# Performance work log

Measured on AMD Instinct MI355X. Metric: run time of the kernel, lower is better.

Reference implementation:

```python
import jax, jax.numpy as jnp
import numpy as np
import math

EPS = 1e-5
GN_GROUPS = 32


def conv2d(x, w, padding):
    # x: [B,C,H,W], w: [O,I,kh,kw]
    return jax.lax.conv_general_dilated(
        x, w, window_strides=(1, 1), padding=[(padding, padding)] * 2,
        dimension_numbers=("NCHW", "OIHW", "NCHW"))


def group_norm(x, weight, bias, groups=GN_GROUPS, eps=EPS):
    B, C, H, W = x.shape
    xg = x.reshape(B, groups, C // groups, H, W)
    mu = xg.mean(axis=(2, 3, 4), keepdims=True)
    var = xg.var(axis=(2, 3, 4), keepdims=True)
    xn = (xg - mu) * jax.lax.rsqrt(var + eps)
    xn = xn.reshape(B, C, H, W)
    return xn * weight[None, :, None, None] + bias[None, :, None, None]


def setup_inputs() -> dict:
    key = jax.random.key(0)
    ks = jax.random.split(key, 8)
    B, C, H, W = 8, 256, 80, 80
    init_gate = 0.99
    gate_bias_val = 0.5 * math.log((1 + init_gate) / (1 - init_gate))
    return {
        "x": jax.random.normal(ks[0], (B, C, H, W), dtype=jnp.float32),
        "w1": jax.random.normal(ks[1], (C, C, 3, 3), dtype=jnp.float32) * 0.01,
        "gn1_w": jnp.ones((C,), dtype=jnp.float32),
        "gn1_b": jnp.zeros((C,), dtype=jnp.float32),
        "w2": jax.random.normal(ks[2], (C, C, 3, 3), dtype=jnp.float32) * 0.01,
        "gn2_w": jnp.ones((C,), dtype=jnp.float32),
        "gn2_b": jnp.zeros((C,), dtype=jnp.float32),
        "gate_w": jax.random.normal(ks[3], (1, C, 1, 1), dtype=jnp.float32) * 0.01,
        "gate_b": jnp.full((1,), gate_bias_val, dtype=jnp.float32),
    }


def reference(x, w1, gn1_w, gn1_b, w2, gn2_w, gn2_b, gate_w, gate_b):
    # shortcut is identity (in_channels == out_channels, stride 1)
    shortcut = x
    # conv1 -> GN -> ReLU
    h = jax.nn.relu(group_norm(conv2d(x, w1, padding=1), gn1_w, gn1_b))
    # conv2 -> GN
    h = group_norm(conv2d(h, w2, padding=1), gn2_w, gn2_b)
    # SpatialGate: 1x1 conv on the original input, ReTanH activation
    g = conv2d(x, gate_w, padding=0) + gate_b[None, :, None, None]  # [B,1,H,W]
    gate = jnp.clip(jnp.tanh(g), 0.0, None)
    # num_groups == 1: encode/decode are identity reshapes; gate broadcasts over C
    out = h * gate
    return jax.nn.relu(out + shortcut)
```

## Files before the change

### kernel.cpp

```cpp
#include <hip/hip_runtime.h>
#include <math.h>

#define NB   8
#define NC   256
#define NH   80
#define NW   80
#define NHW  6400
#define GN_EPS 1e-5f

typedef __bf16 bf16;
typedef bf16 bf16x2 __attribute__((ext_vector_type(2)));
typedef bf16 bf16x4 __attribute__((ext_vector_type(4)));
typedef bf16 bf16x8 __attribute__((ext_vector_type(8)));
typedef float f32x4 __attribute__((ext_vector_type(4)));

typedef __attribute__((address_space(1))) void gvoid;
typedef __attribute__((address_space(3))) void lvoid;
__device__ __forceinline__ void glds16(const void* g, void* l) {
    __builtin_amdgcn_global_load_lds((const gvoid*)g, (lvoid*)l, 16, 0, 0);
}

#define AW_T 2048

#define PREP_GRID 2048

__global__ __launch_bounds__(256) void prep_kernel(
    const float* __restrict__ x, bf16* __restrict__ xp,
    const float* __restrict__ gw, float* __restrict__ gsum,
    const float* __restrict__ w1, const float* __restrict__ w2,
    bf16* __restrict__ wA1, bf16* __restrict__ wA2, float* __restrict__ stats)
{
    int bid = blockIdx.x;
    int tid = threadIdx.x;
    if (bid >= PREP_GRID) {
        int blk = bid - PREP_GRID;
        if (blk == 0) {
            #pragma unroll
            for (int k = 0; k < 8; k++) stats[tid + k * 256] = 0.0f;
            return;
        }
        __shared__ float lw[32 * 292];
        int rb    = blk - 1;
        int wsel  = rb >> 6;
        int chunk = (rb >> 3) & 7;
        int cog   = rb & 7;
        const float* w = wsel ? w2 : w1;
        bf16* wA       = wsel ? wA2 : wA1;
        const float* src = w + (size_t)cog * 32 * 2304 + chunk * 288;
        for (int v = tid; v < 2304; v += 256) {
            int co = v / 72, f4o = v - co * 72;
            float4 t = *(const float4*)(src + (size_t)co * 2304 + f4o * 4);
            *(float4*)(&lw[co * 292 + f4o * 4]) = t;
        }
        __syncthreads();
        for (int v = tid; v < 1152; v += 256) {
            int seg = v >> 6;
            int off = v & 63;
            int tap = seg >> 1, coqL = seg & 1;
            int qq = off >> 4, n = off & 15;
            int coL = coqL * 16 + n;
            bf16x8 pk;
            #pragma unroll
            for (int j = 0; j < 8; j++) {
                int ciL = qq * 8 + j;
                pk[j] = (bf16)lw[coL * 292 + ciL * 9 + tap];
            }
            size_t oidx = (((size_t)(chunk * 9 + tap) * 16 + cog * 2 + coqL) * 512)
                          + qq * 128 + n * 8;
            *(bf16x8*)(wA + oidx) = pk;
        }
        return;
    }
    __shared__ float tile[8][4][88];
    for (int vb = bid; vb < 5120; vb += PREP_GRID) {
        int rg  = vb % 20;
        int cib = (vb / 20) & 31;
        int b   = vb / 640;
        for (int u = tid; u < 640; u += 256) {
            int c8 = u / 80; int rem = u - c8 * 80;
            int rr = rem / 20; int c4 = rem - rr * 20;
            float4 v = *(const float4*)(
                x + ((size_t)(b * NC + cib * 8 + c8) * NH + rg * 4 + rr) * NW + c4 * 4);
            *(float4*)(&tile[c8][rr][c4 * 4]) = v;
        }
        __syncthreads();
        for (int u = tid; u < 320; u += 256) {
            int rr = u / 80, col = u - rr * 80;
            bf16x8 pk;
            #pragma unroll
            for (int j = 0; j < 8; j++) pk[j] = (bf16)tile[j][rr][col];
            size_t base = (((size_t)(b * 32 + cib) * 82 + rg * 4 + rr + 1) * 82) * 8 + 8;
            *(bf16x8*)(xp + base + col * 8) = pk;
        }
        for (int u = tid; u < 320; u += 256) {
            int rr = u / 80, col = u - rr * 80;
            float s = 0.0f;
            #pragma unroll
            for (int c8 = 0; c8 < 8; c8++)
                s = fmaf(tile[c8][rr][col], gw[cib * 8 + c8], s);
            atomicAdd(&gsum[(size_t)b * NHW + (rg * 4 + rr) * 80 + col], s);
        }
        const uint4 z4 = make_uint4(0u, 0u, 0u, 0u);
        size_t img = ((size_t)(b * 32 + cib)) * 82;
        if (tid < 8) {
            int rr = tid >> 1, col = (tid & 1) * 81;
            *(uint4*)(xp + ((img + rg * 4 + rr + 1) * 82 + col) * 8) = z4;
        }
        if (rg == 0 || rg == 19) {
            int prow = (rg == 0) ? 0 : 81;
            for (int u = tid; u < 82; u += 256)
                *(uint4*)(xp + ((img + prow) * 82 + u) * 8) = z4;
        }
        __syncthreads();
    }
}

__global__ __launch_bounds__(256, 4) void conv_kernel(
    const bf16* __restrict__ xp, const bf16* __restrict__ wA,
    bf16* __restrict__ y, float* __restrict__ ssum, float* __restrict__ ssq)
{
    __shared__ __align__(16) bf16 Aw[9 * AW_T];
    __shared__ float wgs[8], wgq[8];

    int tid  = threadIdx.x;
    int wid  = tid >> 6;
    int lane = tid & 63;
    int n = lane & 15, q = lane >> 4;

    int bid = blockIdx.x;
    int ct  = bid / 160;
    int t   = bid - ct * 160;
    int b   = t / 20;
    int rt  = t - b * 20;
    int co0 = ct * 64, h0 = rt * 4;

    if (tid < 8) { wgs[tid] = 0.0f; wgq[tid] = 0.0f; }

    f32x4 acc[4][5];
    #pragma unroll
    for (int i = 0; i < 4; i++)
        #pragma unroll
        for (int j = 0; j < 5; j++) acc[i][j] = (f32x4){0.f, 0.f, 0.f, 0.f};

    for (int c = 0; c < 8; c++) {
        __syncthreads();
        for (int p = wid; p < 36; p += 4) {
            int tap = p >> 2, mt = p & 3;
            glds16((const char*)(wA + (((size_t)c * 9 + tap) * 16 + ct * 4 + mt) * 512) + lane * 16,
                   (char*)(Aw + tap * AW_T + mt * 512) + lane * 16);
        }
        __syncthreads();

        const bf16* awc = Aw + lane * 8;
        const bf16* xq  = xp + (((size_t)(b * 32 + c * 4 + q) * 82 + (h0 + wid)) * 82) * 8 + n * 8;

        bf16x8 L0[15], L1[15];
        #pragma unroll
        for (int k = 0; k < 15; k++)
            L0[k] = *(const bf16x8*)(xq + ((k / 3) * 16 + (k % 3)) * 8);
        #pragma unroll
        for (int k = 0; k < 15; k++)
            L1[k] = *(const bf16x8*)(xq + (82 + (k / 3) * 16 + (k % 3)) * 8);

        #pragma unroll
        for (int s = 0; s < 3; s++) {
            bf16x8 af[4];
            #pragma unroll
            for (int mt = 0; mt < 4; mt++)
                af[mt] = *(const bf16x8*)(awc + s * AW_T + mt * 512);
            #pragma unroll
            for (int mt = 0; mt < 4; mt++)
                #pragma unroll
                for (int nt = 0; nt < 5; nt++)
                    acc[mt][nt] = __builtin_amdgcn_mfma_f32_16x16x32_bf16(
                        af[mt], L0[nt * 3 + s], acc[mt][nt], 0, 0, 0);
        }
        #pragma unroll
        for (int k = 0; k < 15; k++)
            L0[k] = *(const bf16x8*)(xq + (164 + (k / 3) * 16 + (k % 3)) * 8);

        #pragma unroll
        for (int s = 0; s < 3; s++) {
            bf16x8 af[4];
            #pragma unroll
            for (int mt = 0; mt < 4; mt++)
                af[mt] = *(const bf16x8*)(awc + (3 + s) * AW_T + mt * 512);
            #pragma unroll
            for (int mt = 0; mt < 4; mt++)
                #pragma unroll
                for (int nt = 0; nt < 5; nt++)
                    acc[mt][nt] = __builtin_amdgcn_mfma_f32_16x16x32_bf16(
                        af[mt], L1[nt * 3 + s], acc[mt][nt], 0, 0, 0);
        }
        #pragma unroll
        for (int s = 0; s < 3; s++) {
            bf16x8 af[4];
            #pragma unroll
            for (int mt = 0; mt < 4; mt++)
                af[mt] = *(const bf16x8*)(awc + (6 + s) * AW_T + mt * 512);
            #pragma unroll
            for (int mt = 0; mt < 4; mt++)
                #pragma unroll
                for (int nt = 0; nt < 5; nt++)
                    acc[mt][nt] = __builtin_amdgcn_mfma_f32_16x16x32_bf16(
                        af[mt], L0[nt * 3 + s], acc[mt][nt], 0, 0, 0);
        }
    }

    int h = h0 + wid;
    #pragma unroll
    for (int mt = 0; mt < 4; mt++) {
        float s1 = 0.0f, s2 = 0.0f;
        int co  = co0 + mt * 16 + q * 4;
        int cib = co >> 3, c8 = co & 7;
        #pragma unroll
        for (int nt = 0; nt < 5; nt++) {
            int col = nt * 16 + n;
            bf16x4 pk;
            #pragma unroll
            for (int rg = 0; rg < 4; rg++) {
                float v = acc[mt][nt][rg];
                pk[rg] = (bf16)v;
                s1 += v;
                s2 = fmaf(v, v, s2);
            }
            *(bf16x4*)(y + ((((size_t)(b * 32 + cib) * 80 + h) * 80 + col) * 8 + c8)) = pk;
        }
        #pragma unroll
        for (int off = 1; off < 16; off <<= 1) {
            s1 += __shfl_xor(s1, off, 64);
            s2 += __shfl_xor(s2, off, 64);
        }
        if (n == 0) {
            int gl = mt * 2 + (q >> 1);
            atomicAdd(&wgs[gl], s1);
            atomicAdd(&wgq[gl], s2);
        }
    }
    __syncthreads();
    if (tid < 8) {
        atomicAdd(&ssum[b * 32 + ct * 8 + tid], wgs[tid]);
        atomicAdd(&ssq [b * 32 + ct * 8 + tid], wgq[tid]);
    }
}

__global__ __launch_bounds__(256) void prep2_kernel(
    const bf16* __restrict__ y, bf16* __restrict__ xp,
    const float* __restrict__ s, const float* __restrict__ sq,
    const float* __restrict__ gamma, const float* __restrict__ beta)
{
    int bid = blockIdx.x;
    for (int vb = bid; vb < 5120; vb += PREP_GRID) {
        int b = vb / 640; int rem = vb - b * 640;
        int cib = rem / 20; int rq = rem - cib * 20;
        int gidx = b * 32 + cib;
        const float cnt = (float)(8 * NHW);
        float m  = s[gidx] / cnt;
        float vv = sq[gidx] / cnt - m * m;
        float r  = rsqrtf(vv + GN_EPS);
        float scj[8], shj[8];
        #pragma unroll
        for (int j = 0; j < 8; j++) {
            int c = cib * 8 + j;
            scj[j] = r * gamma[c];
            shj[j] = beta[c] - m * scj[j];
        }
        const bf16* src = y + (size_t)(b * 32 + cib) * 51200 + rq * 2560;
        for (int u = threadIdx.x; u < 320; u += 256) {
            int e = u * 8;
            int row = rq * 4 + e / 640;
            int w640 = e - (e / 640) * 640;
            bf16x8 iv = *(const bf16x8*)(src + e);
            bf16x8 pk;
            #pragma unroll
            for (int j = 0; j < 8; j++)
                pk[j] = (bf16)fmaxf(fmaf((float)iv[j], scj[j], shj[j]), 0.0f);
            size_t xidx = (((size_t)(b * 32 + cib) * 82 + row + 1) * 82) * 8 + 8 + w640;
            *(bf16x8*)(xp + xidx) = pk;
        }
    }
}

__global__ __launch_bounds__(256) void final_kernel(
    const bf16* __restrict__ y, const float* __restrict__ x,
    const float* __restrict__ gsum, const float* __restrict__ gb,
    const float* __restrict__ s, const float* __restrict__ sq,
    const float* __restrict__ gamma, const float* __restrict__ beta,
    float* __restrict__ out)
{
    __shared__ float lds[8 * 328];
    int bid = blockIdx.x;
    float gb0 = gb[0];
    for (int vb = bid; vb < 5120; vb += PREP_GRID) {
        int b = vb / 640; int rem = vb - b * 640;
        int cib = rem / 20; int rq = rem - cib * 20;
        int gidx = b * 32 + cib;
        const float cnt = (float)(8 * NHW);
        float m  = s[gidx] / cnt;
        float vv = sq[gidx] / cnt - m * m;
        float r  = rsqrtf(vv + GN_EPS);
        float scj[8], shj[8];
        #pragma unroll
        for (int j = 0; j < 8; j++) {
            int c = cib * 8 + j;
            scj[j] = r * gamma[c];
            shj[j] = beta[c] - m * scj[j];
        }
        const bf16* src = y + (size_t)(b * 32 + cib) * 51200 + rq * 2560;
        for (int u = threadIdx.x; u < 320; u += 256) {
            bf16x8 iv = *(const bf16x8*)(src + u * 8);
            #pragma unroll
            for (int j = 0; j < 8; j++)
                lds[j * 328 + u] = fmaf((float)iv[j], scj[j], shj[j]);
        }
        __syncthreads();
        const float* gp = gsum + (size_t)b * NHW + rq * 320;
        for (int u = threadIdx.x; u < 640; u += 256) {
            int c8 = u / 80; int rc = (u - c8 * 80) * 4;
            int c = cib * 8 + c8;
            size_t oidx = (size_t)(b * NC + c) * NHW + rq * 320 + rc;
            float4 xv = *(const float4*)(x + oidx);
            float4 gv = *(const float4*)(gp + rc);
            float4 lv = *(const float4*)(&lds[c8 * 328 + rc]);
            float4 ov;
            ov.x = fmaxf(fmaf(lv.x, fmaxf(tanhf(gv.x + gb0), 0.0f), xv.x), 0.0f);
            ov.y = fmaxf(fmaf(lv.y, fmaxf(tanhf(gv.y + gb0), 0.0f), xv.y), 0.0f);
            ov.z = fmaxf(fmaf(lv.z, fmaxf(tanhf(gv.z + gb0), 0.0f), xv.z), 0.0f);
            ov.w = fmaxf(fmaf(lv.w, fmaxf(tanhf(gv.w + gb0), 0.0f), xv.w), 0.0f);
            *(float4*)(out + oidx) = ov;
        }
        __syncthreads();
    }
}

extern "C" void kernel_launch(void* const* d_in, const int* in_sizes, int n_in,
                              void* d_out, int out_size, void* d_ws, size_t ws_size,
                              hipStream_t stream)
{
    const float* x     = (const float*)d_in[0];
    const float* w1    = (const float*)d_in[1];
    const float* gn1_w = (const float*)d_in[2];
    const float* gn1_b = (const float*)d_in[3];
    const float* w2    = (const float*)d_in[4];
    const float* gn2_w = (const float*)d_in[5];
    const float* gn2_b = (const float*)d_in[6];
    const float* gw    = (const float*)d_in[7];
    const float* gb    = (const float*)d_in[8];

    bf16*  xp  = (bf16*)d_out;
    float* out = (float*)d_out;

    char* wsb = (char*)d_ws;
    bf16*  y     = (bf16*)wsb;
    float* gsum  = (float*)(wsb + 26214400);
    bf16*  wA1   = (bf16*)(wsb + 26214400 + 204800);
    bf16*  wA2   = wA1 + 589824;
    float* stats = (float*)(wsb + 26214400 + 204800 + 2 * 1179648);
    float* s1  = stats,        * s1q = stats + 256;
    float* s2  = stats + 1024, * s2q = stats + 1280;

    hipMemsetAsync(gsum, 0, NB * NHW * sizeof(float), stream);

    prep_kernel<<<PREP_GRID + 129, 256, 0, stream>>>(x, xp, gw, gsum, w1, w2, wA1, wA2, stats);
    conv_kernel<<<640, 256, 0, stream>>>(xp, wA1, y, s1, s1q);
    prep2_kernel<<<PREP_GRID, 256, 0, stream>>>(y, xp, s1, s1q, gn1_w, gn1_b);
    conv_kernel<<<640, 256, 0, stream>>>(xp, wA2, y, s2, s2q);
    final_kernel<<<PREP_GRID, 256, 0, stream>>>(y, x, gsum, gb, s2, s2q, gn2_w, gn2_b, out);
}
```

Measured before the change: 277.7 us.

## Fuse GroupNorm epilogues into conv kernels using a software grid barrier

Each conv kernel now keeps its accumulators in registers, publishes GroupNorm partial sums, and waits at a device-wide atomic barrier. After the barrier it reads the final statistics and applies the normalization itself. Conv1 writes ReLU(GN) directly into the padded bf16 input buffer for conv2, and conv2 applies GN, the spatial gate, the residual add and the final ReLU straight to the output. This removes the bf16 intermediate tensor and the separate prep2 and final kernels, saving their global-memory round trips and launches. The cost is that all 640 blocks must be resident at once for the barrier, and the final epilogue uses narrower scalar strided stores and loads.

New measurement: 725.4 us. 161% more time.

```diff
diff --git a/kernel.cpp b/kernel.cpp
--- a/kernel.cpp
+++ b/kernel.cpp
@@ -18,6 +18,31 @@
 typedef __attribute__((address_space(3))) void lvoid;
 __device__ __forceinline__ void glds16(const void* g, void* l) {
     __builtin_amdgcn_global_load_lds((const gvoid*)g, (lvoid*)l, 16, 0, 0);
+}
+
+__device__ __forceinline__ void grid_barrier(unsigned* bar, unsigned nblk) {
+    __syncthreads();
+    if (threadIdx.x == 0) {
+        unsigned gen = __hip_atomic_load(&bar[1], __ATOMIC_RELAXED,
+                                         __HIP_MEMORY_SCOPE_AGENT);
+        unsigned prev = __hip_atomic_fetch_add(&bar[0], 1u, __ATOMIC_ACQ_REL,
+                                               __HIP_MEMORY_SCOPE_AGENT);
+        if (prev == nblk - 1u) {
+            __hip_atomic_store(&bar[0], 0u, __ATOMIC_RELAXED,
+                               __HIP_MEMORY_SCOPE_AGENT);
+            __hip_atomic_fetch_add(&bar[1], 1u, __ATOMIC_ACQ_REL,
+                                   __HIP_MEMORY_SCOPE_AGENT);
+        } else {
+            while (__hip_atomic_load(&bar[1], __ATOMIC_ACQUIRE,
+                                     __HIP_MEMORY_SCOPE_AGENT) == gen)
+                __builtin_amdgcn_s_sleep(1);
+        }
+    }
+    __syncthreads();
+}
+
+__device__ __forceinline__ float aload(const float* p) {
+    return __hip_atomic_load(p, __ATOMIC_RELAXED, __HIP_MEMORY_SCOPE_AGENT);
 }
 
 #define AW_T 2048
@@ -115,12 +140,16 @@
     }
 }
 
-__global__ __launch_bounds__(256, 4) void conv_kernel(
-    const bf16* __restrict__ xp, const bf16* __restrict__ wA,
-    bf16* __restrict__ y, float* __restrict__ ssum, float* __restrict__ ssq)
+__global__ __launch_bounds__(256, 4) void conv1_fused(
+    bf16* xp, const bf16* __restrict__ wA,
+    float* __restrict__ ssum, float* __restrict__ ssq,
+    const float* __restrict__ gamma, const float* __restrict__ beta,
+    unsigned* bar)
 {
     __shared__ __align__(16) bf16 Aw[9 * AW_T];
     __shared__ float wgs[8], wgq[8];
+    __shared__ float gm[8], gr[8];
+    __shared__ float lgam[64], lbet[64];
 
     int tid  = threadIdx.x;
     int wid  = tid >> 6;
@@ -135,6 +164,7 @@
     int co0 = ct * 64, h0 = rt * 4;
 
     if (tid < 8) { wgs[tid] = 0.0f; wgq[tid] = 0.0f; }
+    if (tid < 64) { lgam[tid] = gamma[co0 + tid]; lbet[tid] = beta[co0 + tid]; }
 
     f32x4 acc[4][5];
     #pragma unroll
@@ -207,25 +237,17 @@
         }
     }
 
-    int h = h0 + wid;
     #pragma unroll
     for (int mt = 0; mt < 4; mt++) {
         float s1 = 0.0f, s2 = 0.0f;
-        int co  = co0 + mt * 16 + q * 4;
-        int cib = co >> 3, c8 = co & 7;
-        #pragma unroll
-        for (int nt = 0; nt < 5; nt++) {
-            int col = nt * 16 + n;
-            bf16x4 pk;
+        #pragma unroll
+        for (int nt = 0; nt < 5; nt++)
             #pragma unroll
             for (int rg = 0; rg < 4; rg++) {
                 float v = acc[mt][nt][rg];
-                pk[rg] = (bf16)v;
                 s1 += v;
                 s2 = fmaf(v, v, s2);
             }
-            *(bf16x4*)(y + ((((size_t)(b * 32 + cib) * 80 + h) * 80 + col) * 8 + c8)) = pk;
-        }
         #pragma unroll
         for (int off = 1; off < 16; off <<= 1) {
             s1 += __shfl_xor(s1, off, 64);
@@ -242,94 +264,212 @@
         atomicAdd(&ssum[b * 32 + ct * 8 + tid], wgs[tid]);
         atomicAdd(&ssq [b * 32 + ct * 8 + tid], wgq[tid]);
     }
-}
-
-__global__ __launch_bounds__(256) void prep2_kernel(
-    const bf16* __restrict__ y, bf16* __restrict__ xp,
-    const float* __restrict__ s, const float* __restrict__ sq,
-    const float* __restrict__ gamma, const float* __restrict__ beta)
+
+    grid_barrier(bar, 640);
+
+    const float cnt = (float)(8 * NHW);
+    if (tid < 8) {
+        float s  = aload(&ssum[b * 32 + ct * 8 + tid]);
+        float q2 = aload(&ssq [b * 32 + ct * 8 + tid]);
+        float m = s / cnt;
+        gm[tid] = m;
+        gr[tid] = rsqrtf(q2 / cnt - m * m + GN_EPS);
+    }
+    __syncthreads();
+
+    int h = h0 + wid;
+    #pragma unroll
+    for (int mt = 0; mt < 4; mt++) {
+        int gl = mt * 2 + (q >> 1);
+        float m = gm[gl], r = gr[gl];
+        int cL  = mt * 16 + q * 4;
+        int cib = ct * 8 + gl;
+        int c8  = (q * 4) & 7;
+        float sc[4], sh[4];
+        #pragma unroll
+        for (int rg = 0; rg < 4; rg++) {
+            sc[rg] = r * lgam[cL + rg];
+            sh[rg] = lbet[cL + rg] - m * sc[rg];
+        }
+        #pragma unroll
+        for (int nt = 0; nt < 5; nt++) {
+            int col = nt * 16 + n;
+            bf16x4 pk;
+            #pragma unroll
+            for (int rg = 0; rg < 4; rg++)
+                pk[rg] = (bf16)fmaxf(fmaf(acc[mt][nt][rg], sc[rg], sh[rg]), 0.0f);
+            *(bf16x4*)(xp + (((size_t)(b * 32 + cib) * 82 + h + 1) * 82) * 8 + 8 + col * 8 + c8) = pk;
+        }
+    }
+}
+
+__global__ __launch_bounds__(256, 4) void conv2_fused(
+    const bf16* __restrict__ xp, const bf16* __restrict__ wA,
+    const float* __restrict__ x, const float* __restrict__ gsum,
+    const float* __restrict__ gb,
+    float* __restrict__ ssum, float* __restrict__ ssq,
+    const float* __restrict__ gamma, const float* __restrict__ beta,
+    float* __restrict__ out, unsigned* bar)
 {
+    __shared__ __align__(16) bf16 Aw[9 * AW_T];
+    __shared__ float wgs[8], wgq[8];
+    __shared__ float gm[8], gr[8];
+    __shared__ float lgam[64], lbet[64];
+
+    int tid  = threadIdx.x;
+    int wid  = tid >> 6;
+    int lane = tid & 63;
+    int n = lane & 15, q = lane >> 4;
+
     int bid = blockIdx.x;
-    for (int vb = bid; vb < 5120; vb += PREP_GRID) {
-        int b = vb / 640; int rem = vb - b * 640;
-        int cib = rem / 20; int rq = rem - cib * 20;
-        int gidx = b * 32 + cib;
-        const float cnt = (float)(8 * NHW);
-        float m  = s[gidx] / cnt;
-        float vv = sq[gidx] / cnt - m * m;
-        float r  = rsqrtf(vv + GN_EPS);
-        float scj[8], shj[8];
-        #pragma unroll
-        for (int j = 0; j < 8; j++) {
-            int c = cib * 8 + j;
-            scj[j] = r * gamma[c];
-            shj[j] = beta[c] - m * scj[j];
-        }
-        const bf16* src = y + (size_t)(b * 32 + cib) * 51200 + rq * 2560;
-        for (int u = threadIdx.x; u < 320; u += 256) {
-            int e = u * 8;
-            int row = rq * 4 + e / 640;
-            int w640 = e - (e / 640) * 640;
-            bf16x8 iv = *(const bf16x8*)(src + e);
-            bf16x8 pk;
-            #pragma unroll
-            for (int j = 0; j < 8; j++)
-                pk[j] = (bf16)fmaxf(fmaf((float)iv[j], scj[j], shj[j]), 0.0f);
-            size_t xidx = (((size_t)(b * 32 + cib) * 82 + row + 1) * 82) * 8 + 8 + w640;
-            *(bf16x8*)(xp + xidx) = pk;
-        }
-    }
-}
-
-__global__ __launch_bounds__(256) void final_kernel(
-    const bf16* __restrict__ y, const float* __restrict__ x,
-    const float* __restrict__ gsum, const float* __restrict__ gb,
-    const float* __restrict__ s, const float* __restrict__ sq,
-    const float* __restrict__ gamma, const float* __restrict__ beta,
-    float* __restrict__ out)
-{
-    __shared__ float lds[8 * 328];
-    int bid = blockIdx.x;
+    int ct  = bid / 160;
+    int t   = bid - ct * 160;
+    int b   = t / 20;
+    int rt  = t - b * 20;
+    int co0 = ct * 64, h0 = rt * 4;
+
+    if (tid < 8) { wgs[tid] = 0.0f; wgq[tid] = 0.0f; }
+    if (tid < 64) { lgam[tid] = gamma[co0 + tid]; lbet[tid] = beta[co0 + tid]; }
+
+    f32x4 acc[4][5];
+    #pragma unroll
+    for (int i = 0; i < 4; i++)
+        #pragma unroll
+        for (int j = 0; j < 5; j++) acc[i][j] = (f32x4){0.f, 0.f, 0.f, 0.f};
+
+    for (int c = 0; c < 8; c++) {
+        __syncthreads();
+        for (int p = wid; p < 36; p += 4) {
+            int tap = p >> 2, mt = p & 3;
+            glds16((const char*)(wA + (((size_t)c * 9 + tap) * 16 + ct * 4 + mt) * 512) + lane * 16,
+                   (char*)(Aw + tap * AW_T + mt * 512) + lane * 16);
+        }
+        __syncthreads();
+
+        const bf16* awc = Aw + lane * 8;
+        const bf16* xq  = xp + (((size_t)(b * 32 + c * 4 + q) * 82 + (h0 + wid)) * 82) * 8 + n * 8;
+
+        bf16x8 L0[15], L1[15];
+        #pragma unroll
+        for (int k = 0; k < 15; k++)
+            L0[k] = *(const bf16x8*)(xq + ((k / 3) * 16 + (k % 3)) * 8);
+        #pragma unroll
+        for (int k = 0; k < 15; k++)
+            L1[k] = *(const bf16x8*)(xq + (82 + (k / 3) * 16 + (k % 3)) * 8);
+
+        #pragma unroll
+        for (int s = 0; s < 3; s++) {
+            bf16x8 af[4];
+            #pragma unroll
+            for (int mt = 0; mt < 4; mt++)
+                af[mt] = *(const bf16x8*)(awc + s * AW_T + mt * 512);
+            #pragma unroll
+            for (int mt = 0; mt < 4; mt++)
+                #pragma unroll
+                for (int nt = 0; nt < 5; nt++)
+                    acc[mt][nt] = __builtin_amdgcn_mfma_f32_16x16x32_bf16(
+                        af[mt], L0[nt * 3 + s], acc[mt][nt], 0, 0, 0);
+        }
+        #pragma unroll
+        for (int k = 0; k < 15; k++)
+            L0[k] = *(const bf16x8*)(xq + (164 + (k / 3) * 16 + (k % 3)) * 8);
+
+        #pragma unroll
+        for (int s = 0; s < 3; s++) {
+            bf16x8 af[4];
+            #pragma unroll
+            for (int mt = 0; mt < 4; mt++)
+                af[mt] = *(const bf16x8*)(awc + (3 + s) * AW_T + mt * 512);
+            #pragma unroll
+            for (int mt = 0; mt < 4; mt++)
+                #pragma unroll
+                for (int nt = 0; nt < 5; nt++)
+                    acc[mt][nt] = __builtin_amdgcn_mfma_f32_16x16x32_bf16(
+                        af[mt], L1[nt * 3 + s], acc[mt][nt], 0, 0, 0);
+        }
+        #pragma unroll
+        for (int s = 0; s < 3; s++) {
+            bf16x8 af[4];
+            #pragma unroll
+            for (int mt = 0; mt < 4; mt++)
+                af[mt] = *(const bf16x8*)(awc + (6 + s) * AW_T + mt * 512);
+            #pragma unroll
+            for (int mt = 0; mt < 4; mt++)
+                #pragma unroll
+                for (int nt = 0; nt < 5; nt++)
+                    acc[mt][nt] = __builtin_amdgcn_mfma_f32_16x16x32_bf16(
+                        af[mt], L0[nt * 3 + s], acc[mt][nt], 0, 0, 0);
+        }
+    }
+
+    #pragma unroll
+    for (int mt = 0; mt < 4; mt++) {
+        float s1 = 0.0f, s2 = 0.0f;
+        #pragma unroll
+        for (int nt = 0; nt < 5; nt++)
+            #pragma unroll
+            for (int rg = 0; rg < 4; rg++) {
+                float v = acc[mt][nt][rg];
+                s1 += v;
+                s2 = fmaf(v, v, s2);
+            }
+        #pragma unroll
+        for (int off = 1; off < 16; off <<= 1) {
+            s1 += __shfl_xor(s1, off, 64);
+            s2 += __shfl_xor(s2, off, 64);
+        }
+        if (n == 0) {
+            int gl = mt * 2 + (q >> 1);
+            atomicAdd(&wgs[gl], s1);
+            atomicAdd(&wgq[gl], s2);
+        }
+    }
+    __syncthreads();
+    if (tid < 8) {
+        atomicAdd(&ssum[b * 32 + ct * 8 + tid], wgs[tid]);
+        atomicAdd(&ssq [b * 32 + ct * 8 + tid], wgq[tid]);
+    }
+
+    grid_barrier(bar, 640);
+
+    const float cnt = (float)(8 * NHW);
+    if (tid < 8) {
+        float s  = aload(&ssum[b * 32 + ct * 8 + tid]);
+        float q2 = aload(&ssq [b * 32 + ct * 8 + tid]);
+        float m = s / cnt;
+        gm[tid] = m;
+        gr[tid] = rsqrtf(q2 / cnt - m * m + GN_EPS);
+    }
+    __syncthreads();
+
+    int h = h0 + wid;
     float gb0 = gb[0];
-    for (int vb = bid; vb < 5120; vb += PREP_GRID) {
-        int b = vb / 640; int rem = vb - b * 640;
-        int cib = rem / 20; int rq = rem - cib * 20;
-        int gidx = b * 32 + cib;
-        const float cnt = (float)(8 * NHW);
-        float m  = s[gidx] / cnt;
-        float vv = sq[gidx] / cnt - m * m;
-        float r  = rsqrtf(vv + GN_EPS);
-        float scj[8], shj[8];
-        #pragma unroll
-        for (int j = 0; j < 8; j++) {
-            int c = cib * 8 + j;
-            scj[j] = r * gamma[c];
-            shj[j] = beta[c] - m * scj[j];
-        }
-        const bf16* src = y + (size_t)(b * 32 + cib) * 51200 + rq * 2560;
-        for (int u = threadIdx.x; u < 320; u += 256) {
-            bf16x8 iv = *(const bf16x8*)(src + u * 8);
-            #pragma unroll
-            for (int j = 0; j < 8; j++)
-                lds[j * 328 + u] = fmaf((float)iv[j], scj[j], shj[j]);
-        }
-        __syncthreads();
-        const float* gp = gsum + (size_t)b * NHW + rq * 320;
-        for (int u = threadIdx.x; u < 640; u += 256) {
-            int c8 = u / 80; int rc = (u - c8 * 80) * 4;
-            int c = cib * 8 + c8;
-            size_t oidx = (size_t)(b * NC + c) * NHW + rq * 320 + rc;
-            float4 xv = *(const float4*)(x + oidx);
-            float4 gv = *(const float4*)(gp + rc);
-            float4 lv = *(const float4*)(&lds[c8 * 328 + rc]);
-            float4 ov;
-            ov.x = fmaxf(fmaf(lv.x, fmaxf(tanhf(gv.x + gb0), 0.0f), xv.x), 0.0f);
-            ov.y = fmaxf(fmaf(lv.y, fmaxf(tanhf(gv.y + gb0), 0.0f), xv.y), 0.0f);
-            ov.z = fmaxf(fmaf(lv.z, fmaxf(tanhf(gv.z + gb0), 0.0f), xv.z), 0.0f);
-            ov.w = fmaxf(fmaf(lv.w, fmaxf(tanhf(gv.w + gb0), 0.0f), xv.w), 0.0f);
-            *(float4*)(out + oidx) = ov;
-        }
-        __syncthreads();
+    float gatev[5];
+    #pragma unroll
+    for (int nt = 0; nt < 5; nt++)
+        gatev[nt] = fmaxf(tanhf(gsum[(size_t)b * NHW + h * 80 + nt * 16 + n] + gb0), 0.0f);
+    #pragma unroll
+    for (int mt = 0; mt < 4; mt++) {
+        int gl = mt * 2 + (q >> 1);
+        float m = gm[gl], r = gr[gl];
+        int cL = mt * 16 + q * 4;
+        float sc[4], sh[4];
+        #pragma unroll
+        for (int rg = 0; rg < 4; rg++) {
+            sc[rg] = r * lgam[cL + rg];
+            sh[rg] = lbet[cL + rg] - m * sc[rg];
+        }
+        #pragma unroll
+        for (int nt = 0; nt < 5; nt++) {
+            int col = nt * 16 + n;
+            #pragma unroll
+            for (int rg = 0; rg < 4; rg++) {
+                int c = co0 + cL + rg;
+                size_t oidx = (size_t)(b * NC + c) * NHW + h * 80 + col;
+                float v = fmaf(acc[mt][nt][rg], sc[rg], sh[rg]);
+                out[oidx] = fmaxf(fmaf(v, gatev[nt], x[oidx]), 0.0f);
+            }
+        }
     }
 }
 
@@ -351,19 +491,18 @@
     float* out = (float*)d_out;
 
     char* wsb = (char*)d_ws;
-    bf16*  y     = (bf16*)wsb;
     float* gsum  = (float*)(wsb + 26214400);
     bf16*  wA1   = (bf16*)(wsb + 26214400 + 204800);
     bf16*  wA2   = wA1 + 589824;
     float* stats = (float*)(wsb + 26214400 + 204800 + 2 * 1179648);
     float* s1  = stats,        * s1q = stats + 256;
     float* s2  = stats + 1024, * s2q = stats + 1280;
+    unsigned* bar1 = (unsigned*)(stats + 1792);
+    unsigned* bar2 = (unsigned*)(stats + 1800);
 
     hipMemsetAsync(gsum, 0, NB * NHW * sizeof(float), stream);
 
     prep_kernel<<<PREP_GRID + 129, 256, 0, stream>>>(x, xp, gw, gsum, w1, w2, wA1, wA2, stats);
-    conv_kernel<<<640, 256, 0, stream>>>(xp, wA1, y, s1, s1q);
-    prep2_kernel<<<PREP_GRID, 256, 0, stream>>>(y, xp, s1, s1q, gn1_w, gn1_b);
-    conv_kernel<<<640, 256, 0, stream>>>(xp, wA2, y, s2, s2q);
-    final_kernel<<<PREP_GRID, 256, 0, stream>>>(y, x, gsum, gb, s2, s2q, gn2_w, gn2_b, out);
-}
+    conv1_fused<<<640, 256, 0, stream>>>(xp, wA1, s1, s1q, gn1_w, gn1_b, bar1);
+    conv2_fused<<<640, 256, 0, stream>>>(xp, wA2, x, gsum, gb, s2, s2q, gn2_w, gn2_b, out, bar2);
+}
```
